# Kernel tuning notes

Measured on AMD Instinct MI355X. Metric: run time of the kernel, lower is better.

## Reference

```python
import jax, jax.numpy as jnp
import numpy as np

NEG_SLOPE = 0.2
EPS = 1e-16  # PyG softmax denominator epsilon


def gatv2_layer(x, src, dst, W_l, W_r, att, bias, num_nodes, heads, out_dim, concat):
    # x: [N, F_in]; src/dst: [E] (self-loops already included)
    x_l = (x @ W_l).reshape(num_nodes, heads, out_dim)  # source transform
    x_r = (x @ W_r).reshape(num_nodes, heads, out_dim)  # target transform
    # GATv2 scoring: a^T LeakyReLU(x_l[j] + x_r[i])
    e = jax.nn.leaky_relu(x_l[src] + x_r[dst], NEG_SLOPE)       # [E, H, D]
    logits = jnp.einsum('ehd,hd->eh', e, att)                    # [E, H]
    # segment softmax over incoming edges of each target node
    m = jax.ops.segment_max(logits, dst, num_segments=num_nodes)  # [N, H]
    ex = jnp.exp(logits - m[dst])                                 # [E, H]
    denom = jax.ops.segment_sum(ex, dst, num_segments=num_nodes)  # [N, H]
    alpha = ex / (denom[dst] + EPS)                               # [E, H]
    msg = x_l[src] * alpha[:, :, None]                            # [E, H, D]
    out = jax.ops.segment_sum(msg, dst, num_segments=num_nodes)   # [N, H, D]
    if concat:
        out = out.reshape(num_nodes, heads * out_dim)
    else:
        out = out.mean(axis=1)
    return out + bias


def setup_inputs() -> dict:
    key = jax.random.key(0)
    ks = jax.random.split(key, 10)
    N, E, F_in, H, D, F_out = 50000, 400000, 256, 4, 128, 64

    def glorot(k, shape, fan):
        return jax.random.normal(k, shape, dtype=jnp.float32) * (1.0 / np.sqrt(fan))

    return {
        'x': jax.random.normal(ks[0], (N, F_in), dtype=jnp.float32),
        'edge_index': jax.random.randint(ks[1], (2, E), 0, N, dtype=jnp.int64),
        'W_l1': glorot(ks[2], (F_in, H * D), F_in),
        'W_r1': glorot(ks[3], (F_in, H * D), F_in),
        'att1': glorot(ks[4], (H, D), D),
        'b1': jnp.zeros((H * D,), dtype=jnp.float32),
        'W_l2': glorot(ks[5], (H * D, F_out), H * D),
        'W_r2': glorot(ks[6], (H * D, F_out), H * D),
        'att2': glorot(ks[7], (1, F_out), F_out),
        'b2': jnp.zeros((F_out,), dtype=jnp.float32),
    }


def reference(x, edge_index, W_l1, W_r1, att1, b1, W_l2, W_r2, att2, b2):
    N = x.shape[0]
    # add self-loops (PyG GATv2Conv default add_self_loops=True)
    loops = jnp.arange(N, dtype=edge_index.dtype)
    src = jnp.concatenate([edge_index[0], loops])
    dst = jnp.concatenate([edge_index[1], loops])
    # dropout(p=0.6) is identity in eval mode
    h = gatv2_layer(x, src, dst, W_l1, W_r1, att1, b1, N, heads=4, out_dim=128, concat=True)
    h = jax.nn.elu(h)
    out = gatv2_layer(h, src, dst, W_l2, W_r2, att2, b2, N, heads=1, out_dim=64, concat=False)
    return out
```

## Files before the change

### kernel.cpp

```cpp
#include <hip/hip_runtime.h>
#include <hip/hip_bf16.h>
#include <math.h>


#define NEG_SLOPE 0.2f

typedef _Float16 half8 __attribute__((ext_vector_type(8)));
typedef _Float16 h2 __attribute__((ext_vector_type(2)));
typedef float f32x4 __attribute__((ext_vector_type(4)));

#if __has_builtin(__builtin_amdgcn_global_load_lds)
#define HAS_GLL 1
__device__ __forceinline__ void gll16(const _Float16* g, _Float16* l) {
    __builtin_amdgcn_global_load_lds(
        (const __attribute__((address_space(1))) unsigned int*)g,
        (__attribute__((address_space(3))) unsigned int*)l, 16, 0, 0);
}
#endif

__device__ __forceinline__ float dot2acc(h2 a, h2 b, float c) {
#if __has_builtin(__builtin_amdgcn_fdot2)
    return __builtin_amdgcn_fdot2(a, b, c, false);
#else
    return fmaf((float)a[1], (float)b[1], fmaf((float)a[0], (float)b[0], c));
#endif
}


__global__ __launch_bounds__(256) void k_castx_count(const float* __restrict__ x, _Float16* __restrict__ xh,
                                                     int n8, const int* __restrict__ ei,
                                                     int* __restrict__ counts, int E, int Etot, int gEtot) {
    int b = blockIdx.x;
    if (b < gEtot) {
        int i = b * 256 + threadIdx.x;
        if (i < Etot) {
            int dst = (i < E) ? ei[E + i] : (i - E);
            atomicAdd(&counts[dst], 1);
        }
    } else {
        int i = (b - gEtot) * 256 + threadIdx.x;
        if (i < n8) {
            const float4* p = (const float4*)(x + i * 8);
            float4 a = p[0], c = p[1];
            half8 v;
            v[0] = (_Float16)a.x; v[1] = (_Float16)a.y; v[2] = (_Float16)a.z; v[3] = (_Float16)a.w;
            v[4] = (_Float16)c.x; v[5] = (_Float16)c.y; v[6] = (_Float16)c.z; v[7] = (_Float16)c.w;
            *(half8*)(xh + i * 8) = v;
        }
    }
}


__global__ __launch_bounds__(1024) void k_castw_scana(const int* __restrict__ counts, int* __restrict__ offs,
                                                      int* __restrict__ partial, int n, int nsb,
                                                      const float* __restrict__ Wl1, const float* __restrict__ Wr1,
                                                      const float* __restrict__ Wl2, const float* __restrict__ Wr2,
                                                      _Float16* __restrict__ W1T, _Float16* __restrict__ W2T) {
    __shared__ int buf[1024];
    int b = blockIdx.x, t = threadIdx.x;
    if (b < nsb) {
        int i = b * 1024 + t;
        int v = (i < n) ? counts[i] : 0;
        buf[t] = v;
        __syncthreads();
        #pragma unroll
        for (int off = 1; off < 1024; off <<= 1) {
            int add = (t >= off) ? buf[t - off] : 0;
            __syncthreads();
            buf[t] += add;
            __syncthreads();
        }
        if (i < n) offs[i + 1] = buf[t];
        if (t == 1023) partial[b] = buf[1023];
    } else {
        int i = (b - nsb) * 1024 + t;
        const int T1 = 1024 * 256;
        const int T2 = 128 * 512;
        if (i < T1) {
            int nn = i >> 8, k = i & 255;
            float v = (nn < 512) ? Wl1[k * 512 + nn] : Wr1[k * 512 + (nn - 512)];
            W1T[i] = (_Float16)v;
        } else if (i < T1 + T2) {
            int j = i - T1;
            int nn = j >> 9, k = j & 511;
            float v = (nn < 64) ? Wl2[k * 64 + nn] : Wr2[k * 64 + (nn - 64)];
            W2T[j] = (_Float16)v;
        }
    }
}

__global__ __launch_bounds__(1024) void k_scan_b(int* __restrict__ partial, int nb) {
    __shared__ int buf[1024];
    int t = threadIdx.x;
    int v = (t < nb) ? partial[t] : 0;
    buf[t] = v;
    __syncthreads();
    #pragma unroll
    for (int off = 1; off < 1024; off <<= 1) {
        int add = (t >= off) ? buf[t - off] : 0;
        __syncthreads();
        buf[t] += add;
        __syncthreads();
    }
    if (t < nb) partial[t] = buf[t] - v;
}

__global__ __launch_bounds__(256) void k_scan_c(int* __restrict__ offs, int* __restrict__ cursor,
                                                const int* __restrict__ partial, int n) {
    int i = blockIdx.x * 256 + threadIdx.x;
    if (i == 0) { offs[0] = 0; cursor[0] = 0; }
    if (i < n) {
        int v = offs[i + 1] + partial[i >> 10];
        offs[i + 1] = v;
        cursor[i + 1] = v;
    }
}

__global__ __launch_bounds__(256) void k_fill(const int* __restrict__ ei, int* __restrict__ cursor,
                                              int* __restrict__ csr_src, int E, int Etot) {
    int i = blockIdx.x * 256 + threadIdx.x;
    if (i >= Etot) return;
    int src, dst;
    if (i < E) { src = ei[i]; dst = ei[E + i]; }
    else       { src = i - E; dst = i - E; }
    int pos = atomicAdd(&cursor[dst], 1);
    csr_src[pos] = src;
}


__global__ __launch_bounds__(256) void k_gemm_f16(const _Float16* __restrict__ A,
                                                  const _Float16* __restrict__ Bt,
                                                  _Float16* __restrict__ C,
                                                  int M, int N, int K, int ntiles) {
    __shared__ _Float16 As[128 * 32];
    __shared__ _Float16 Bs[128 * 32];

    int tid = threadIdx.x;
    int lane = tid & 63;
    int wave = tid >> 6;
    int wm = wave >> 1, wn = wave & 1;
    int l15 = lane & 15, q = lane >> 4;

    int ntile = blockIdx.x % ntiles;
    int mtile = blockIdx.x / ntiles;
    int tileM = mtile * 128;
    int tileN = ntile * 128;

    int srow = lane >> 2;
    int schunk = (lane & 3) ^ ((lane >> 3) & 3);
    const _Float16* gA0 = A + (long)(tileM + wave * 32 + srow) * K + schunk * 8;
    const _Float16* gA1 = gA0 + (long)16 * K;
    const _Float16* gB0 = Bt + (long)(tileN + wave * 32 + srow) * K + schunk * 8;
    const _Float16* gB1 = gB0 + (long)16 * K;
    _Float16* lA0 = As + wave * 1024;
    _Float16* lA1 = lA0 + 512;
    _Float16* lB0 = Bs + wave * 1024;
    _Float16* lB1 = lB0 + 512;

    int aswz = (q ^ ((l15 >> 1) & 3)) * 8;

    f32x4 acc[4][4];
    #pragma unroll
    for (int i = 0; i < 4; ++i)
        #pragma unroll
        for (int j = 0; j < 4; ++j)
            acc[i][j] = (f32x4)(0.f);

    for (int k0 = 0; k0 < K; k0 += 32) {
#ifdef HAS_GLL
        gll16(gA0 + k0, lA0);
        gll16(gA1 + k0, lA1);
        gll16(gB0 + k0, lB0);
        gll16(gB1 + k0, lB1);
#else
        half8 va0 = *(const half8*)(gA0 + k0);
        half8 va1 = *(const half8*)(gA1 + k0);
        half8 vb0 = *(const half8*)(gB0 + k0);
        half8 vb1 = *(const half8*)(gB1 + k0);
        *(half8*)(lA0 + lane * 8) = va0;
        *(half8*)(lA1 + lane * 8) = va1;
        *(half8*)(lB0 + lane * 8) = vb0;
        *(half8*)(lB1 + lane * 8) = vb1;
#endif
        __syncthreads();

        half8 af[4], bf[4];
        #pragma unroll
        for (int i = 0; i < 4; ++i)
            af[i] = *(const half8*)(As + (wm * 64 + i * 16 + l15) * 32 + aswz);
        #pragma unroll
        for (int j = 0; j < 4; ++j)
            bf[j] = *(const half8*)(Bs + (wn * 64 + j * 16 + l15) * 32 + aswz);
        #pragma unroll
        for (int i = 0; i < 4; ++i)
            #pragma unroll
            for (int j = 0; j < 4; ++j)
                acc[i][j] = __builtin_amdgcn_mfma_f32_16x16x32_f16(af[i], bf[j], acc[i][j], 0, 0, 0);
        __syncthreads();
    }

    #pragma unroll
    for (int i = 0; i < 4; ++i) {
        #pragma unroll
        for (int r = 0; r < 4; ++r) {
            int grow = tileM + wm * 64 + i * 16 + q * 4 + r;
            if (grow < M) {
                #pragma unroll
                for (int j = 0; j < 4; ++j) {
                    int gcol = tileN + wn * 64 + j * 16 + l15;
                    C[(long)grow * N + gcol] = (_Float16)acc[i][j][r];
                }
            }
        }
    }
}


__global__ __launch_bounds__(256) void k_attn1(const _Float16* __restrict__ xlr,
                                               const float* __restrict__ att, const float* __restrict__ b1,
                                               const int* __restrict__ offs, const int* __restrict__ csr_src,
                                               _Float16* __restrict__ hout, int N) {
    int wave = threadIdx.x >> 6;
    int lane = threadIdx.x & 63;
    int node = blockIdx.x * 4 + wave;
    if (node >= N) return;

    int eh = lane >> 5;
    int hl = lane & 31;
    int cbase = (hl >> 3) * 128 + (hl & 7) * 16;

    half8 xra = *(const half8*)(xlr + (long)node * 1024 + 512 + cbase);
    half8 xrb = *(const half8*)(xlr + (long)node * 1024 + 512 + cbase + 8);
    h2 xr[8], at[8];
    #pragma unroll
    for (int j = 0; j < 4; ++j) {
        xr[j][0] = xra[2 * j];     xr[j][1] = xra[2 * j + 1];
        xr[4 + j][0] = xrb[2 * j]; xr[4 + j][1] = xrb[2 * j + 1];
    }
    #pragma unroll
    for (int j = 0; j < 8; ++j) {
        at[j][0] = (_Float16)att[cbase + 2 * j];
        at[j][1] = (_Float16)att[cbase + 2 * j + 1];
    }
    const h2 ns2 = {(_Float16)NEG_SLOPE, (_Float16)NEG_SLOPE};

    float l = 0.f;
    float acc[16] = {};

    int e0 = offs[node], e1 = offs[node + 1];
    int e = e0 + eh;
    half8 c0, c1;
    if (e < e1) {
        int s = csr_src[e];
        c0 = *(const half8*)(xlr + (long)s * 1024 + cbase);
        c1 = *(const half8*)(xlr + (long)s * 1024 + cbase + 8);
    }
    while (e < e1) {
        half8 u0 = c0, u1 = c1;
        int en = e + 2;
        if (en < e1) {
            int s = csr_src[en];
            c0 = *(const half8*)(xlr + (long)s * 1024 + cbase);
            c1 = *(const half8*)(xlr + (long)s * 1024 + cbase + 8);
        }
        const h2* up = (const h2*)&u0;
        const h2* vp = (const h2*)&u1;
        float p = 0.f;
        #pragma unroll
        for (int j = 0; j < 4; ++j) {
            h2 t = up[j] + xr[j];
#if __has_builtin(__builtin_elementwise_max)
            t = __builtin_elementwise_max(t, t * ns2);
#else
            h2 tn = t * ns2;
            t[0] = (t[0] > tn[0]) ? t[0] : tn[0];
            t[1] = (t[1] > tn[1]) ? t[1] : tn[1];
#endif
            p = dot2acc(t, at[j], p);
        }
        #pragma unroll
        for (int j = 0; j < 4; ++j) {
            h2 t = vp[j] + xr[4 + j];
#if __has_builtin(__builtin_elementwise_max)
            t = __builtin_elementwise_max(t, t * ns2);
#else
            h2 tn = t * ns2;
            t[0] = (t[0] > tn[0]) ? t[0] : tn[0];
            t[1] = (t[1] > tn[1]) ? t[1] : tn[1];
#endif
            p = dot2acc(t, at[4 + j], p);
        }
        p += __shfl_xor(p, 1, 64);
        p += __shfl_xor(p, 2, 64);
        p += __shfl_xor(p, 4, 64);
        float w = __expf(p);
        l += w;
        #pragma unroll
        for (int j = 0; j < 8; ++j) acc[j] = fmaf(w, (float)u0[j], acc[j]);
        #pragma unroll
        for (int j = 0; j < 8; ++j) acc[8 + j] = fmaf(w, (float)u1[j], acc[8 + j]);
        e = en;
    }

    l += __shfl_xor(l, 32, 64);
    #pragma unroll
    for (int j = 0; j < 16; ++j) acc[j] += __shfl_xor(acc[j], 32, 64);

    if (eh == 0) {
        float inv = 1.f / (l + 1e-16f);
        half8 o0, o1;
        #pragma unroll
        for (int j = 0; j < 8; ++j) {
            float o = fmaf(acc[j], inv, b1[cbase + j]);
            o = (o > 0.f) ? o : (__expf(o) - 1.f);
            o0[j] = (_Float16)o;
        }
        #pragma unroll
        for (int j = 0; j < 8; ++j) {
            float o = fmaf(acc[8 + j], inv, b1[cbase + 8 + j]);
            o = (o > 0.f) ? o : (__expf(o) - 1.f);
            o1[j] = (_Float16)o;
        }
        *(half8*)(hout + (long)node * 512 + cbase) = o0;
        *(half8*)(hout + (long)node * 512 + cbase + 8) = o1;
    }
}


__global__ __launch_bounds__(256) void k_attn2(const _Float16* __restrict__ xlr2,
                                               const float* __restrict__ att, const float* __restrict__ b2,
                                               const int* __restrict__ offs, const int* __restrict__ csr_src,
                                               float* __restrict__ out, int N) {
    int wave = threadIdx.x >> 6;
    int lane = threadIdx.x & 63;
    int node = blockIdx.x * 4 + wave;
    if (node >= N) return;

    int eh = lane >> 5;
    int hl = lane & 31;
    int ch = hl * 2;

    h2 xrh = *(const h2*)(xlr2 + (long)node * 128 + 64 + ch);
    h2 ath; ath[0] = (_Float16)att[ch]; ath[1] = (_Float16)att[ch + 1];
    const h2 ns2 = {(_Float16)NEG_SLOPE, (_Float16)NEG_SLOPE};

    float l = 0.f, a0 = 0.f, a1 = 0.f;
    int e0 = offs[node], e1 = offs[node + 1];
    int e = e0 + eh;
    h2 cv;
    if (e < e1) {
        int s = csr_src[e];
        cv = *(const h2*)(xlr2 + (long)s * 128 + ch);
    }
    while (e < e1) {
        h2 u = cv;
        int en = e + 2;
        if (en < e1) {
            int s = csr_src[en];
            cv = *(const h2*)(xlr2 + (long)s * 128 + ch);
        }
        h2 t = u + xrh;
#if __has_builtin(__builtin_elementwise_max)
        t = __builtin_elementwise_max(t, t * ns2);
#else
        h2 tn = t * ns2;
        t[0] = (t[0] > tn[0]) ? t[0] : tn[0];
        t[1] = (t[1] > tn[1]) ? t[1] : tn[1];
#endif
        float p = dot2acc(t, ath, 0.f);
        p += __shfl_xor(p, 1, 64);
        p += __shfl_xor(p, 2, 64);
        p += __shfl_xor(p, 4, 64);
        p += __shfl_xor(p, 8, 64);
        p += __shfl_xor(p, 16, 64);
        float w = __expf(p);
        l += w;
        a0 = fmaf(w, (float)u[0], a0);
        a1 = fmaf(w, (float)u[1], a1);
        e = en;
    }
    l += __shfl_xor(l, 32, 64);
    a0 += __shfl_xor(a0, 32, 64);
    a1 += __shfl_xor(a1, 32, 64);
    if (eh == 0) {
        float inv = 1.f / (l + 1e-16f);
        float2 o;
        o.x = fmaf(a0, inv, b2[ch]);
        o.y = fmaf(a1, inv, b2[ch + 1]);
        *(float2*)(out + (long)node * 64 + ch) = o;
    }
}


extern "C" void kernel_launch(void* const* d_in, const int* in_sizes, int n_in,
                              void* d_out, int out_size, void* d_ws, size_t ws_size,
                              hipStream_t stream) {
    const float* x    = (const float*)d_in[0];
    const int*   ei   = (const int*)d_in[1];
    const float* Wl1  = (const float*)d_in[2];
    const float* Wr1  = (const float*)d_in[3];
    const float* att1 = (const float*)d_in[4];
    const float* b1   = (const float*)d_in[5];
    const float* Wl2  = (const float*)d_in[6];
    const float* Wr2  = (const float*)d_in[7];
    const float* att2 = (const float*)d_in[8];
    const float* b2   = (const float*)d_in[9];
    float* out = (float*)d_out;

    const int F_IN = 256;
    int N = in_sizes[0] / F_IN;
    int E = in_sizes[1] / 2;
    int Etot = E + N;
    int nScanBlocks = (N + 1023) / 1024;
    int mtiles = (N + 127) / 128;
    int Mpad = mtiles * 128;

    char* p = (char*)d_ws;
    auto carve = [&](size_t bytes) -> void* {
        void* r = (void*)p;
        p += (bytes + 255) & ~(size_t)255;
        return r;
    };
    _Float16* xh   = (_Float16*)carve((size_t)Mpad * 256 * 2);
    _Float16* W1T  = (_Float16*)carve((size_t)1024 * 256 * 2);
    _Float16* W2T  = (_Float16*)carve((size_t)128 * 512 * 2);
    _Float16* C1   = (_Float16*)carve((size_t)N * 1024 * 2);
    _Float16* h    = (_Float16*)carve((size_t)Mpad * 512 * 2);
    _Float16* C2   = (_Float16*)carve((size_t)N * 128 * 2);
    int* counts  = (int*)carve((size_t)N * 4);
    int* offs    = (int*)carve((size_t)(N + 1) * 4);
    int* cursor  = (int*)carve((size_t)(N + 1) * 4);
    int* partial = (int*)carve((size_t)nScanBlocks * 4);
    int* csr     = (int*)carve((size_t)Etot * 4);

    int gN    = (N + 255) / 256;
    int gEtot = (Etot + 255) / 256;
    int n8    = N * 256 / 8;
    int gCast = (n8 + 255) / 256;

    hipMemsetAsync(counts, 0, (size_t)N * 4, stream);

    k_castx_count<<<gEtot + gCast, 256, 0, stream>>>(x, xh, n8, ei, counts, E, Etot, gEtot);

    {
        int total = 1024 * 256 + 128 * 512;
        int gW = (total + 1023) / 1024;
        k_castw_scana<<<nScanBlocks + gW, 1024, 0, stream>>>(counts, offs, partial, N, nScanBlocks,
                                                             Wl1, Wr1, Wl2, Wr2, W1T, W2T);
    }
    k_scan_b<<<1, 1024, 0, stream>>>(partial, nScanBlocks);
    k_scan_c<<<gN, 256, 0, stream>>>(offs, cursor, partial, N);
    k_fill<<<gEtot, 256, 0, stream>>>(ei, cursor, csr, E, Etot);

    k_gemm_f16<<<mtiles * 8, 256, 0, stream>>>(xh, W1T, C1, N, 1024, 256, 8);
    k_attn1<<<(N + 3) / 4, 256, 0, stream>>>(C1, att1, b1, offs, csr, h, N);

    k_gemm_f16<<<mtiles, 256, 0, stream>>>(h, W2T, C2, N, 128, 512, 1);
    k_attn2<<<(N + 3) / 4, 256, 0, stream>>>(C2, att2, b2, offs, csr, out, N);
}
```

Baseline: 348.1 us.

## Fuse scan stages, merge CSR fill into GEMM1, restructure attn1 per-wave edges

Merges the two-stage partial-sum scan into one kernel where every block redundantly scans the block partials, and folds the CSR fill into the first GEMM launch as extra blocks, cutting launch count and serialization. attn1 now has one wave process a node's edges sequentially with 8 channels per lane instead of splitting edges across half-waves, which removes the cross-half reduction. Both attention kernels prescale att by log2(e) and use a native exp2. The redundant per-block scan assumes at most 256 scan blocks, and the serial edge loop gives less memory-level parallelism per wave.

```diff
diff --git a/kernel.cpp b/kernel.cpp
--- a/kernel.cpp
+++ b/kernel.cpp
@@ -4,6 +4,7 @@
 
 
 #define NEG_SLOPE 0.2f
+#define LOG2E 1.4426950408889634f
 
 typedef _Float16 half8 __attribute__((ext_vector_type(8)));
 typedef _Float16 h2 __attribute__((ext_vector_type(2)));
@@ -23,6 +24,14 @@
     return __builtin_amdgcn_fdot2(a, b, c, false);
 #else
     return fmaf((float)a[1], (float)b[1], fmaf((float)a[0], (float)b[0], c));
+#endif
+}
+
+__device__ __forceinline__ float fast_exp2(float p) {
+#if __has_builtin(__builtin_amdgcn_exp2f)
+    return __builtin_amdgcn_exp2f(p);
+#else
+    return exp2f(p);
 #endif
 }
 
@@ -89,60 +98,47 @@
     }
 }
 
-__global__ __launch_bounds__(1024) void k_scan_b(int* __restrict__ partial, int nb) {
-    __shared__ int buf[1024];
+
+__global__ __launch_bounds__(256) void k_scanbc(int* __restrict__ offs, int* __restrict__ cursor,
+                                                const int* __restrict__ partial, int n, int nsb) {
+    __shared__ int s[256];
     int t = threadIdx.x;
-    int v = (t < nb) ? partial[t] : 0;
-    buf[t] = v;
+    int v = (t < nsb) ? partial[t] : 0;
+    s[t] = v;
     __syncthreads();
     #pragma unroll
-    for (int off = 1; off < 1024; off <<= 1) {
-        int add = (t >= off) ? buf[t - off] : 0;
+    for (int off = 1; off < 256; off <<= 1) {
+        int add = (t >= off) ? s[t - off] : 0;
         __syncthreads();
-        buf[t] += add;
+        s[t] += add;
         __syncthreads();
     }
-    if (t < nb) partial[t] = buf[t] - v;
-}
-
-__global__ __launch_bounds__(256) void k_scan_c(int* __restrict__ offs, int* __restrict__ cursor,
-                                                const int* __restrict__ partial, int n) {
-    int i = blockIdx.x * 256 + threadIdx.x;
+    int excl = s[t] - v;
+    s[t] = excl;
+    __syncthreads();
+    int i = blockIdx.x * 256 + t;
     if (i == 0) { offs[0] = 0; cursor[0] = 0; }
     if (i < n) {
-        int v = offs[i + 1] + partial[i >> 10];
-        offs[i + 1] = v;
-        cursor[i + 1] = v;
-    }
-}
-
-__global__ __launch_bounds__(256) void k_fill(const int* __restrict__ ei, int* __restrict__ cursor,
-                                              int* __restrict__ csr_src, int E, int Etot) {
-    int i = blockIdx.x * 256 + threadIdx.x;
-    if (i >= Etot) return;
-    int src, dst;
-    if (i < E) { src = ei[i]; dst = ei[E + i]; }
-    else       { src = i - E; dst = i - E; }
-    int pos = atomicAdd(&cursor[dst], 1);
-    csr_src[pos] = src;
-}
-
-
-__global__ __launch_bounds__(256) void k_gemm_f16(const _Float16* __restrict__ A,
-                                                  const _Float16* __restrict__ Bt,
-                                                  _Float16* __restrict__ C,
-                                                  int M, int N, int K, int ntiles) {
-    __shared__ _Float16 As[128 * 32];
-    __shared__ _Float16 Bs[128 * 32];
-
+        int w = offs[i + 1] + s[i >> 10];
+        offs[i + 1] = w;
+        cursor[i + 1] = w;
+    }
+}
+
+
+__device__ __forceinline__ void gemm_body(const _Float16* __restrict__ A,
+                                          const _Float16* __restrict__ Bt,
+                                          _Float16* __restrict__ C,
+                                          int M, int N, int K, int ntiles, int blk,
+                                          _Float16* As, _Float16* Bs) {
     int tid = threadIdx.x;
     int lane = tid & 63;
     int wave = tid >> 6;
     int wm = wave >> 1, wn = wave & 1;
     int l15 = lane & 15, q = lane >> 4;
 
-    int ntile = blockIdx.x % ntiles;
-    int mtile = blockIdx.x / ntiles;
+    int ntile = blk % ntiles;
+    int mtile = blk / ntiles;
     int tileM = mtile * 128;
     int tileN = ntile * 128;
 
@@ -215,6 +211,38 @@
     }
 }
 
+__global__ __launch_bounds__(256) void k_gemm1_fill(const _Float16* __restrict__ A,
+                                                    const _Float16* __restrict__ Bt,
+                                                    _Float16* __restrict__ C,
+                                                    int M, int N, int K, int ntiles, int gb,
+                                                    const int* __restrict__ ei, int* __restrict__ cursor,
+                                                    int* __restrict__ csr_src, int E, int Etot) {
+    __shared__ _Float16 As[128 * 32];
+    __shared__ _Float16 Bs[128 * 32];
+    int b = blockIdx.x;
+    if (b < gb) {
+        gemm_body(A, Bt, C, M, N, K, ntiles, b, As, Bs);
+    } else {
+        int i = (b - gb) * 256 + threadIdx.x;
+        if (i < Etot) {
+            int src, dst;
+            if (i < E) { src = ei[i]; dst = ei[E + i]; }
+            else       { src = i - E; dst = i - E; }
+            int pos = atomicAdd(&cursor[dst], 1);
+            csr_src[pos] = src;
+        }
+    }
+}
+
+__global__ __launch_bounds__(256) void k_gemm_f16(const _Float16* __restrict__ A,
+                                                  const _Float16* __restrict__ Bt,
+                                                  _Float16* __restrict__ C,
+                                                  int M, int N, int K, int ntiles) {
+    __shared__ _Float16 As[128 * 32];
+    __shared__ _Float16 Bs[128 * 32];
+    gemm_body(A, Bt, C, M, N, K, ntiles, blockIdx.x, As, Bs);
+}
+
 
 __global__ __launch_bounds__(256) void k_attn1(const _Float16* __restrict__ xlr,
                                                const float* __restrict__ att, const float* __restrict__ b1,
@@ -225,50 +253,41 @@
     int node = blockIdx.x * 4 + wave;
     if (node >= N) return;
 
-    int eh = lane >> 5;
-    int hl = lane & 31;
-    int cbase = (hl >> 3) * 128 + (hl & 7) * 16;
-
-    half8 xra = *(const half8*)(xlr + (long)node * 1024 + 512 + cbase);
-    half8 xrb = *(const half8*)(xlr + (long)node * 1024 + 512 + cbase + 8);
-    h2 xr[8], at[8];
+    int cbase = (lane >> 4) * 128 + (lane & 15) * 8;
+
+    half8 xrv8 = *(const half8*)(xlr + (long)node * 1024 + 512 + cbase);
+    float4 atv0 = *(const float4*)(att + cbase);
+    float4 atv1 = *(const float4*)(att + cbase + 4);
+    h2 xr[4], at[4];
     #pragma unroll
     for (int j = 0; j < 4; ++j) {
-        xr[j][0] = xra[2 * j];     xr[j][1] = xra[2 * j + 1];
-        xr[4 + j][0] = xrb[2 * j]; xr[4 + j][1] = xrb[2 * j + 1];
-    }
-    #pragma unroll
-    for (int j = 0; j < 8; ++j) {
-        at[j][0] = (_Float16)att[cbase + 2 * j];
-        at[j][1] = (_Float16)att[cbase + 2 * j + 1];
-    }
+        xr[j][0] = xrv8[2 * j]; xr[j][1] = xrv8[2 * j + 1];
+    }
+    at[0][0] = (_Float16)(atv0.x * LOG2E); at[0][1] = (_Float16)(atv0.y * LOG2E);
+    at[1][0] = (_Float16)(atv0.z * LOG2E); at[1][1] = (_Float16)(atv0.w * LOG2E);
+    at[2][0] = (_Float16)(atv1.x * LOG2E); at[2][1] = (_Float16)(atv1.y * LOG2E);
+    at[3][0] = (_Float16)(atv1.z * LOG2E); at[3][1] = (_Float16)(atv1.w * LOG2E);
     const h2 ns2 = {(_Float16)NEG_SLOPE, (_Float16)NEG_SLOPE};
 
     float l = 0.f;
-    float acc[16] = {};
+    float acc[8] = {};
 
     int e0 = offs[node], e1 = offs[node + 1];
-    int e = e0 + eh;
-    half8 c0, c1;
-    if (e < e1) {
-        int s = csr_src[e];
-        c0 = *(const half8*)(xlr + (long)s * 1024 + cbase);
-        c1 = *(const half8*)(xlr + (long)s * 1024 + cbase + 8);
-    }
-    while (e < e1) {
-        half8 u0 = c0, u1 = c1;
-        int en = e + 2;
-        if (en < e1) {
-            int s = csr_src[en];
-            c0 = *(const half8*)(xlr + (long)s * 1024 + cbase);
-            c1 = *(const half8*)(xlr + (long)s * 1024 + cbase + 8);
-        }
-        const h2* up = (const h2*)&u0;
-        const h2* vp = (const h2*)&u1;
+    int s_next = csr_src[e0];
+    int s_next2 = (e0 + 1 < e1) ? csr_src[e0 + 1] : 0;
+    half8 xlv = *(const half8*)(xlr + (long)s_next * 1024 + cbase);
+
+    for (int e = e0; e < e1; ++e) {
+        half8 cur = xlv;
+        int s_pf = s_next2;
+        if (e + 2 < e1) s_next2 = csr_src[e + 2];
+        if (e + 1 < e1) xlv = *(const half8*)(xlr + (long)s_pf * 1024 + cbase);
+
+        const h2* cp = (const h2*)&cur;
         float p = 0.f;
         #pragma unroll
         for (int j = 0; j < 4; ++j) {
-            h2 t = up[j] + xr[j];
+            h2 t = cp[j] + xr[j];
 #if __has_builtin(__builtin_elementwise_max)
             t = __builtin_elementwise_max(t, t * ns2);
 #else
@@ -279,51 +298,25 @@
             p = dot2acc(t, at[j], p);
         }
         #pragma unroll
-        for (int j = 0; j < 4; ++j) {
-            h2 t = vp[j] + xr[4 + j];
-#if __has_builtin(__builtin_elementwise_max)
-            t = __builtin_elementwise_max(t, t * ns2);
-#else
-            h2 tn = t * ns2;
-            t[0] = (t[0] > tn[0]) ? t[0] : tn[0];
-            t[1] = (t[1] > tn[1]) ? t[1] : tn[1];
-#endif
-            p = dot2acc(t, at[4 + j], p);
-        }
-        p += __shfl_xor(p, 1, 64);
-        p += __shfl_xor(p, 2, 64);
-        p += __shfl_xor(p, 4, 64);
-        float w = __expf(p);
+        for (int off = 1; off <= 8; off <<= 1) p += __shfl_xor(p, off, 64);
+        float w = fast_exp2(p);
         l += w;
         #pragma unroll
-        for (int j = 0; j < 8; ++j) acc[j] = fmaf(w, (float)u0[j], acc[j]);
-        #pragma unroll
-        for (int j = 0; j < 8; ++j) acc[8 + j] = fmaf(w, (float)u1[j], acc[8 + j]);
-        e = en;
-    }
-
-    l += __shfl_xor(l, 32, 64);
+        for (int j = 0; j < 8; ++j) acc[j] = fmaf(w, (float)cur[j], acc[j]);
+    }
+
+    float inv = 1.f / (l + 1e-16f);
+    float4 b1v0 = *(const float4*)(b1 + cbase);
+    float4 b1v1 = *(const float4*)(b1 + cbase + 4);
+    float bb[8] = {b1v0.x, b1v0.y, b1v0.z, b1v0.w, b1v1.x, b1v1.y, b1v1.z, b1v1.w};
+    half8 ov;
     #pragma unroll
-    for (int j = 0; j < 16; ++j) acc[j] += __shfl_xor(acc[j], 32, 64);
-
-    if (eh == 0) {
-        float inv = 1.f / (l + 1e-16f);
-        half8 o0, o1;
-        #pragma unroll
-        for (int j = 0; j < 8; ++j) {
-            float o = fmaf(acc[j], inv, b1[cbase + j]);
-            o = (o > 0.f) ? o : (__expf(o) - 1.f);
-            o0[j] = (_Float16)o;
-        }
-        #pragma unroll
-        for (int j = 0; j < 8; ++j) {
-            float o = fmaf(acc[8 + j], inv, b1[cbase + 8 + j]);
-            o = (o > 0.f) ? o : (__expf(o) - 1.f);
-            o1[j] = (_Float16)o;
-        }
-        *(half8*)(hout + (long)node * 512 + cbase) = o0;
-        *(half8*)(hout + (long)node * 512 + cbase + 8) = o1;
-    }
+    for (int j = 0; j < 8; ++j) {
+        float o = fmaf(acc[j], inv, bb[j]);
+        o = (o > 0.f) ? o : (__expf(o) - 1.f);
+        ov[j] = (_Float16)o;
+    }
+    *(half8*)(hout + (long)node * 512 + cbase) = ov;
 }
 
 
@@ -341,7 +334,8 @@
     int ch = hl * 2;
 
     h2 xrh = *(const h2*)(xlr2 + (long)node * 128 + 64 + ch);
-    h2 ath; ath[0] = (_Float16)att[ch]; ath[1] = (_Float16)att[ch + 1];
+    float2 atf = *(const float2*)(att + ch);
+    h2 ath; ath[0] = (_Float16)(atf.x * LOG2E); ath[1] = (_Float16)(atf.y * LOG2E);
     const h2 ns2 = {(_Float16)NEG_SLOPE, (_Float16)NEG_SLOPE};
 
     float l = 0.f, a0 = 0.f, a1 = 0.f;
@@ -373,7 +367,7 @@
         p += __shfl_xor(p, 4, 64);
         p += __shfl_xor(p, 8, 64);
         p += __shfl_xor(p, 16, 64);
-        float w = __expf(p);
+        float w = fast_exp2(p);
         l += w;
         a0 = fmaf(w, (float)u[0], a0);
         a1 = fmaf(w, (float)u[1], a1);
@@ -448,11 +442,13 @@
         k_castw_scana<<<nScanBlocks + gW, 1024, 0, stream>>>(counts, offs, partial, N, nScanBlocks,
                                                              Wl1, Wr1, Wl2, Wr2, W1T, W2T);
     }
-    k_scan_b<<<1, 1024, 0, stream>>>(partial, nScanBlocks);
-    k_scan_c<<<gN, 256, 0, stream>>>(offs, cursor, partial, N);
-    k_fill<<<gEtot, 256, 0, stream>>>(ei, cursor, csr, E, Etot);
-
-    k_gemm_f16<<<mtiles * 8, 256, 0, stream>>>(xh, W1T, C1, N, 1024, 256, 8);
+    k_scanbc<<<gN, 256, 0, stream>>>(offs, cursor, partial, N, nScanBlocks);
+
+    {
+        int gb = mtiles * 8;
+        k_gemm1_fill<<<gb + gEtot, 256, 0, stream>>>(xh, W1T, C1, N, 1024, 256, 8, gb,
+                                                     ei, cursor, csr, E, Etot);
+    }
     k_attn1<<<(N + 3) / 4, 256, 0, stream>>>(C1, att1, b1, offs, csr, h, N);
 
     k_gemm_f16<<<mtiles, 256, 0, stream>>>(h, W2T, C2, N, 128, 512, 1);
```

Result: faster. 334.1 us (-4.0%).
